# Optimization experiments

Measured on AMD Instinct MI355X. Metric: run time of the kernel, lower is better.

The kernel has to match this reference:

```python
import jax, jax.numpy as jnp
import numpy as np

SEQ, D_IN, D_OUT = 4096, 1024, 1024

def setup_inputs() -> dict:
    key = jax.random.key(0)
    kx, kq, kk, kv = jax.random.split(key, 4)
    s = 1.0 / np.sqrt(D_IN)
    return {
        "x": jax.random.normal(kx, (SEQ, D_IN), dtype=jnp.float32),
        "Wq": jax.random.uniform(kq, (D_IN, D_OUT), dtype=jnp.float32, minval=-s, maxval=s),
        "Wk": jax.random.uniform(kk, (D_IN, D_OUT), dtype=jnp.float32, minval=-s, maxval=s),
        "Wv": jax.random.uniform(kv, (D_IN, D_OUT), dtype=jnp.float32, minval=-s, maxval=s),
    }

def reference(x, Wq, Wk, Wv):
    # Single-head self-attention on a 2-D input [S, d_in].
    q = x @ Wq  # [S, d_out]
    k = x @ Wk
    v = x @ Wv
    scale = 1.0 / jnp.sqrt(jnp.asarray(k.shape[-1], dtype=q.dtype))
    attn = jax.nn.softmax(jnp.einsum('sd,td->st', q, k) * scale, axis=-1)  # [S, S]
    return attn @ v  # [S, d_out]
```

## Files before the change

kernel.cpp:

```cpp
#include <hip/hip_runtime.h>
#include <stdint.h>

typedef __bf16 bf16;
typedef __bf16 bf16x8 __attribute__((ext_vector_type(8)));
typedef __bf16 bf16x4 __attribute__((ext_vector_type(4)));
typedef float  f32x4  __attribute__((ext_vector_type(4)));

#define DEVINL __device__ __forceinline__

DEVINL void gload_lds16(const void* g, void* l) {
  __builtin_amdgcn_global_load_lds(
      (const __attribute__((address_space(1))) uint32_t*)g,
      (__attribute__((address_space(3))) uint32_t*)l, 16, 0, 0);
}

DEVINL void swizzle_xy(int& bx, int& by) {
  const int gx = gridDim.x, gy = gridDim.y;
  const int nwg = gx * gy;
  int lin = blockIdx.y * gx + blockIdx.x;
  if ((nwg & 7) == 0) lin = (lin & 7) * (nwg >> 3) + (lin >> 3);
  bx = lin % gx; by = lin / gx;
}

template<int SWM>
DEVINL int swz(int r) { return ((r ^ (r >> 2)) & SWM) << 4; }

template<int BM, int BN, int BK>
DEVINL void gemm_core(const bf16* __restrict__ A, const bf16* __restrict__ Bt,
                      int K, int row0, int col0,
                      bf16* As, bf16* Bs, f32x4 (&acc)[BM/32][BN/32])
{
  constexpr int FM = BM / 32, FN = BN / 32;
  constexpr int RB  = BK * 2;
  constexpr int SWM = (RB / 16) - 1 > 7 ? 7 : (RB / 16) - 1;
  constexpr int IA  = BM * RB / 4096;
  constexpr int IB  = BN * RB / 4096;
  constexpr int RPI = 4096 / RB;
  constexpr int ABY = BM * BK * 2;
  constexpr int BBY = BN * BK * 2;
  const int tid = threadIdx.x;
  const int wave = tid >> 6, lane = tid & 63;

  const int sL   = tid * 16;
  const int srow = sL / RB;
  const int scb  = (sL % RB) ^ swz<SWM>(srow);
  const bf16* gA = A  + (size_t)(row0 + srow) * K + (scb >> 1);
  const bf16* gB = Bt + (size_t)(col0 + srow) * K + (scb >> 1);

  const int wr = (wave >> 1) * (BM / 2);
  const int wc = (wave & 1)  * (BN / 2);
  const int fr = lane & 15, kg16 = (lane >> 4) * 16;

  #pragma unroll
  for (int i = 0; i < FM; i++)
    #pragma unroll
    for (int j = 0; j < FN; j++)
      acc[i][j] = f32x4{0.f, 0.f, 0.f, 0.f};

  auto stage = [&](int buf, int ti) {
    const bf16* ga = gA + (size_t)ti * BK;
    const bf16* gb = gB + (size_t)ti * BK;
    #pragma unroll
    for (int i = 0; i < IA; i++)
      gload_lds16(ga + (size_t)i * RPI * K, (char*)As + buf * ABY + i * 4096 + sL);
    #pragma unroll
    for (int i = 0; i < IB; i++)
      gload_lds16(gb + (size_t)i * RPI * K, (char*)Bs + buf * BBY + i * 4096 + sL);
  };

  const int nt = K / BK;
  stage(0, 0);
  __syncthreads();
  int cur = 0;
  for (int ti = 0; ti < nt; ++ti) {
    if (ti + 1 < nt) stage(cur ^ 1, ti + 1);
    const char* aB = (const char*)As + cur * ABY;
    const char* bB = (const char*)Bs + cur * BBY;
    #pragma unroll
    for (int kk = 0; kk < BK / 32; ++kk) {
      bf16x8 af[FM], bg[FN];
      #pragma unroll
      for (int m = 0; m < FM; m++) {
        const int r = wr + fr + m * 16;
        af[m] = *(const bf16x8*)(aB + r * RB + ((kk * 64 + kg16) ^ swz<SWM>(r)));
      }
      #pragma unroll
      for (int n = 0; n < FN; n++) {
        const int r = wc + fr + n * 16;
        bg[n] = *(const bf16x8*)(bB + r * RB + ((kk * 64 + kg16) ^ swz<SWM>(r)));
      }
      #pragma unroll
      for (int m = 0; m < FM; m++)
        #pragma unroll
        for (int n = 0; n < FN; n++)
          acc[m][n] = __builtin_amdgcn_mfma_f32_16x16x32_bf16(af[m], bg[n], acc[m][n], 0, 0, 0);
    }
    __syncthreads();
    cur ^= 1;
  }
}

template<int BM, int BN, int BK, int MODE>
__global__ __launch_bounds__(256)
void gemm_bt(const bf16* __restrict__ A, const bf16* __restrict__ Bt,
             void* __restrict__ Cout, int K, int ldc)
{
  __shared__ __align__(16) bf16 As[2 * BM * BK];
  __shared__ __align__(16) bf16 Bs[2 * BN * BK];
  int bx, by; swizzle_xy(bx, by);
  const int row0 = by * BM, col0 = bx * BN;
  f32x4 acc[BM / 32][BN / 32];
  gemm_core<BM, BN, BK>(A, Bt, K, row0, col0, As, Bs, acc);

  const int wave = threadIdx.x >> 6, lane = threadIdx.x & 63;
  const int wr = (wave >> 1) * (BM / 2), wc = (wave & 1) * (BN / 2);
  const int ec = lane & 15, er = (lane >> 4) * 4;
  #pragma unroll
  for (int m = 0; m < BM / 32; m++)
    #pragma unroll
    for (int n = 0; n < BN / 32; n++) {
      const int r = row0 + wr + m * 16 + er;
      const int c = col0 + wc + n * 16 + ec;
      if constexpr (MODE == 0) {
        bf16* C = (bf16*)Cout;
        #pragma unroll
        for (int j = 0; j < 4; j++)
          C[(size_t)(r + j) * ldc + c] = (bf16)acc[m][n][j];
      } else {
        float* C = (float*)Cout;
        #pragma unroll
        for (int j = 0; j < 4; j++)
          C[(size_t)(r + j) * ldc + c] = acc[m][n][j];
      }
    }
}

__global__ __launch_bounds__(256)
void gemm_qkv(const bf16* __restrict__ xb, const bf16* __restrict__ Wt,
              bf16* __restrict__ Qb, bf16* __restrict__ Kb, bf16* __restrict__ Vt)
{
  __shared__ __align__(16) bf16 As[2 * 128 * 32];
  __shared__ __align__(16) bf16 Bs[2 * 128 * 32];
  const int z = blockIdx.z;
  int bx, by; swizzle_xy(bx, by);
  const int row0 = by * 128, col0 = bx * 128;
  f32x4 acc[4][4];
  gemm_core<128, 128, 32>(xb, Wt + (size_t)z * 1024 * 1024, 1024, row0, col0, As, Bs, acc);

  const int wave = threadIdx.x >> 6, lane = threadIdx.x & 63;
  const int wr = (wave >> 1) * 64, wc = (wave & 1) * 64;
  const int ec = lane & 15, er = (lane >> 4) * 4;
  if (z == 2) {
    #pragma unroll
    for (int m = 0; m < 4; m++)
      #pragma unroll
      for (int n = 0; n < 4; n++) {
        const int r = row0 + wr + m * 16 + er;
        const int c = col0 + wc + n * 16 + ec;
        bf16x4 pk;
        #pragma unroll
        for (int j = 0; j < 4; j++) pk[j] = (bf16)acc[m][n][j];
        *(bf16x4*)(Vt + (size_t)c * 4096 + r) = pk;
      }
  } else {
    bf16* C = z ? Kb : Qb;
    const float sc = z ? 1.0f : 0.03125f;
    #pragma unroll
    for (int m = 0; m < 4; m++)
      #pragma unroll
      for (int n = 0; n < 4; n++) {
        const int r = row0 + wr + m * 16 + er;
        const int c = col0 + wc + n * 16 + ec;
        #pragma unroll
        for (int j = 0; j < 4; j++)
          C[(size_t)(r + j) * 1024 + c] = (bf16)(acc[m][n][j] * sc);
      }
  }
}

__global__ __launch_bounds__(256)
void softmax_inplace(bf16* __restrict__ S)
{
  const int t = threadIdx.x;
  bf16* p = S + (size_t)blockIdx.x * 4096 + t * 16;
  bf16x8 v0 = *(const bf16x8*)p;
  bf16x8 v1 = *(const bf16x8*)(p + 8);
  float f[16];
  #pragma unroll
  for (int j = 0; j < 8; j++) { f[j] = (float)v0[j]; f[8 + j] = (float)v1[j]; }
  float mx = f[0];
  #pragma unroll
  for (int j = 1; j < 16; j++) mx = fmaxf(mx, f[j]);
  #pragma unroll
  for (int off = 32; off > 0; off >>= 1) mx = fmaxf(mx, __shfl_xor(mx, off));
  __shared__ float rmax[4], rsum[4];
  const int wave = t >> 6, lane = t & 63;
  if (lane == 0) rmax[wave] = mx;
  __syncthreads();
  mx = fmaxf(fmaxf(rmax[0], rmax[1]), fmaxf(rmax[2], rmax[3]));
  float s = 0.f;
  #pragma unroll
  for (int j = 0; j < 16; j++) { f[j] = __expf(f[j] - mx); s += f[j]; }
  #pragma unroll
  for (int off = 32; off > 0; off >>= 1) s += __shfl_xor(s, off);
  if (lane == 0) rsum[wave] = s;
  __syncthreads();
  const float inv = 1.f / (rsum[0] + rsum[1] + rsum[2] + rsum[3]);
  #pragma unroll
  for (int j = 0; j < 8; j++) {
    v0[j] = (bf16)(f[j] * inv);
    v1[j] = (bf16)(f[8 + j] * inv);
  }
  *(bf16x8*)p = v0;
  *(bf16x8*)(p + 8) = v1;
}

__global__ __launch_bounds__(256)
void cvt_f32_bf16(const float* __restrict__ in, bf16* __restrict__ o)
{
  const size_t i = ((size_t)blockIdx.x * 256 + threadIdx.x) * 8;
  const float4 a = *(const float4*)(in + i);
  const float4 b = *(const float4*)(in + i + 4);
  bf16x8 v;
  v[0] = (bf16)a.x; v[1] = (bf16)a.y; v[2] = (bf16)a.z; v[3] = (bf16)a.w;
  v[4] = (bf16)b.x; v[5] = (bf16)b.y; v[6] = (bf16)b.z; v[7] = (bf16)b.w;
  *(bf16x8*)(o + i) = v;
}

__global__ __launch_bounds__(256)
void transpose_cvt(const float* __restrict__ Wq, const float* __restrict__ Wk,
                   const float* __restrict__ Wv, bf16* __restrict__ Wt)
{
  const float* W = blockIdx.z == 0 ? Wq : (blockIdx.z == 1 ? Wk : Wv);
  bf16* O = Wt + (size_t)blockIdx.z * 1024 * 1024;
  __shared__ bf16 tile[64][65];
  const int tx = threadIdx.x & 63;
  const int tg = threadIdx.x >> 6;
  const int r0 = blockIdx.y * 64;
  const int c0 = blockIdx.x * 64;
  #pragma unroll
  for (int i = 0; i < 16; i++) {
    const int r = i * 4 + tg;
    tile[tx][r] = (bf16)W[(size_t)(r0 + r) * 1024 + c0 + tx];
  }
  __syncthreads();
  #pragma unroll
  for (int i = 0; i < 16; i++) {
    const int rr = i * 4 + tg;
    O[(size_t)(c0 + rr) * 1024 + r0 + tx] = tile[rr][tx];
  }
}

extern "C" void kernel_launch(void* const* d_in, const int* in_sizes, int n_in,
                              void* d_out, int out_size, void* d_ws, size_t ws_size,
                              hipStream_t stream)
{
  const float* x  = (const float*)d_in[0];
  const float* Wq = (const float*)d_in[1];
  const float* Wk = (const float*)d_in[2];
  const float* Wv = (const float*)d_in[3];
  char* ws = (char*)d_ws;
  const size_t MB = 1024 * 1024;
  bf16* xb = (bf16*)(ws);
  bf16* Wt = (bf16*)(ws +  8 * MB);
  bf16* Qb = (bf16*)(ws + 14 * MB);
  bf16* Kb = (bf16*)(ws + 22 * MB);
  bf16* Vt = (bf16*)(ws + 30 * MB);
  bf16* S  = (bf16*)(ws + 38 * MB);

  cvt_f32_bf16   <<<dim3(2048),      dim3(256), 0, stream>>>(x, xb);
  transpose_cvt  <<<dim3(16, 16, 3), dim3(256), 0, stream>>>(Wq, Wk, Wv, Wt);
  gemm_qkv       <<<dim3(8, 32, 3),  dim3(256), 0, stream>>>(xb, Wt, Qb, Kb, Vt);
  gemm_bt<128, 128, 32, 0><<<dim3(32, 32), dim3(256), 0, stream>>>(Qb, Kb, (void*)S, 1024, 4096);
  softmax_inplace<<<dim3(4096),      dim3(256), 0, stream>>>(S);
  gemm_bt<128, 64, 64, 1><<<dim3(16, 32), dim3(256), 0, stream>>>(S, Vt, (void*)d_out, 4096, 1024);
}
```

Baseline: 221.9 us.

## Use 256x256-tile 8-wave pipelined GEMM for QKV projection and QK^T

Adds a new GEMM core with 256x256 output tiles, 512 threads (8 waves), K-tile 64, and a double-buffered direct-to-LDS load schedule. The per-half loads are interleaved with four MFMA quadrant phases, separated by explicit barriers and s_setprio. The QKV projection and the Q·K^T score GEMM both switch to this kernel, and QKV is launched as one 12x16 grid over the concatenated weights. The aim is more data reuse per tile and overlap of global loads with MFMA work. The cost is far fewer workgroups (192 and 256) plus heavy register and 128KB LDS use, which can leave CUs underfilled.

```diff
diff --git a/kernel.cpp b/kernel.cpp
--- a/kernel.cpp
+++ b/kernel.cpp
@@ -7,6 +7,8 @@
 typedef float  f32x4  __attribute__((ext_vector_type(4)));
 
 #define DEVINL __device__ __forceinline__
+#define BAR()    asm volatile("s_barrier" ::: "memory")
+#define WAITV(n) asm volatile("s_waitcnt vmcnt(" #n ")" ::: "memory")
 
 DEVINL void gload_lds16(const void* g, void* l) {
   __builtin_amdgcn_global_load_lds(
@@ -20,6 +22,166 @@
   int lin = blockIdx.y * gx + blockIdx.x;
   if ((nwg & 7) == 0) lin = (lin & 7) * (nwg >> 3) + (lin >> 3);
   bx = lin % gx; by = lin / gx;
+}
+
+DEVINL void gemm8_core(const bf16* __restrict__ A, const bf16* __restrict__ Bt,
+                       int row0, int col0, char* Asm, char* Bsm,
+                       f32x4 (&acc)[8][4])
+{
+  const int t = threadIdx.x;
+  const int wave = t >> 6, lane = t & 63;
+  const int wm = wave >> 2, wn = wave & 3;
+  const int wmBase = wm * 128, wnBase = wn * 64;
+  const int fr = lane & 15, kg16 = (lane >> 4) * 16;
+  const int fsw = (fr & 7) << 4;
+
+  const int sL   = t * 16;
+  const int srow = t >> 3;
+  const int scb  = ((t & 7) << 4) ^ ((srow & 7) << 4);
+  const bf16* Ag = A  + (size_t)(row0 + srow) * 1024 + (scb >> 1);
+  const bf16* Bg = Bt + (size_t)(col0 + srow) * 1024 + (scb >> 1);
+
+  bf16x8 aF[4][2], bF[4][2];
+
+  #pragma unroll
+  for (int i = 0; i < 8; i++)
+    #pragma unroll
+    for (int j = 0; j < 4; j++)
+      acc[i][j] = f32x4{0.f, 0.f, 0.f, 0.f};
+
+  auto stA = [&](int buf, int kt2, int h) {
+    const bf16* g = Ag + (size_t)h * 131072 + kt2 * 64;
+    char* l = Asm + buf * 32768 + h * 16384 + sL;
+    gload_lds16(g, l);
+    gload_lds16(g + 65536, l + 8192);
+  };
+  auto stB = [&](int buf, int kt2, int h) {
+    const bf16* g = Bg + (size_t)h * 131072 + kt2 * 64;
+    char* l = Bsm + buf * 32768 + h * 16384 + sL;
+    gload_lds16(g, l);
+    gload_lds16(g + 65536, l + 8192);
+  };
+  auto rdA = [&](const char* cA, int qm) {
+    #pragma unroll
+    for (int m = 0; m < 4; m++)
+      #pragma unroll
+      for (int kk = 0; kk < 2; kk++)
+        aF[m][kk] = *(const bf16x8*)(cA + (wmBase + qm * 64 + m * 16 + fr) * 128
+                                        + (((kk << 6) + kg16) ^ fsw));
+  };
+  auto rdB = [&](const char* cB, int qn) {
+    #pragma unroll
+    for (int n = 0; n < 2; n++)
+      #pragma unroll
+      for (int kk = 0; kk < 2; kk++)
+        bF[qn * 2 + n][kk] = *(const bf16x8*)(cB + (wnBase + qn * 32 + n * 16 + fr) * 128
+                                                 + (((kk << 6) + kg16) ^ fsw));
+  };
+  auto quad = [&](int qm, int qn) {
+    #pragma unroll
+    for (int m = 0; m < 4; m++)
+      #pragma unroll
+      for (int n = 0; n < 2; n++)
+        #pragma unroll
+        for (int kk = 0; kk < 2; kk++)
+          acc[qm * 4 + m][qn * 2 + n] = __builtin_amdgcn_mfma_f32_16x16x32_bf16(
+              aF[m][kk], bF[qn * 2 + n][kk], acc[qm * 4 + m][qn * 2 + n], 0, 0, 0);
+  };
+
+  stB(0, 0, 0); stA(0, 0, 0); stA(0, 0, 1); stB(0, 0, 1);
+  stB(1, 1, 0); stA(1, 1, 0);
+  WAITV(4); BAR();
+
+  #pragma unroll 1
+  for (int kt = 0; kt < 16; ++kt) {
+    const int cur = kt & 1, oth = cur ^ 1;
+    const char* cA = Asm + cur * 32768;
+    const char* cB = Bsm + cur * 32768;
+    rdA(cA, 0); rdB(cB, 0);
+    if (kt + 1 < 16) stA(oth, kt + 1, 1);
+    BAR(); __builtin_amdgcn_s_setprio(1); quad(0, 0); __builtin_amdgcn_s_setprio(0); BAR();
+    rdB(cB, 1);
+    if (kt + 1 < 16) stB(oth, kt + 1, 1);
+    BAR(); __builtin_amdgcn_s_setprio(1); quad(0, 1); __builtin_amdgcn_s_setprio(0); BAR();
+    rdA(cA, 1);
+    if (kt + 2 < 16) stB(cur, kt + 2, 0);
+    BAR(); __builtin_amdgcn_s_setprio(1); quad(1, 1); __builtin_amdgcn_s_setprio(0); BAR();
+    if (kt + 2 < 16) stA(cur, kt + 2, 0);
+    BAR(); __builtin_amdgcn_s_setprio(1); quad(1, 0); __builtin_amdgcn_s_setprio(0);
+    if (kt < 14)       { WAITV(4); }
+    else if (kt == 14) { WAITV(0); }
+    BAR();
+  }
+}
+
+__global__ __launch_bounds__(512, 2)
+void gemm8_s(const bf16* __restrict__ Qb, const bf16* __restrict__ Kb,
+             bf16* __restrict__ S)
+{
+  __shared__ __align__(16) char Asm[65536];
+  __shared__ __align__(16) char Bsm[65536];
+  int bx, by; swizzle_xy(bx, by);
+  const int row0 = by * 256, col0 = bx * 256;
+  f32x4 acc[8][4];
+  gemm8_core(Qb, Kb, row0, col0, Asm, Bsm, acc);
+
+  const int wave = threadIdx.x >> 6, lane = threadIdx.x & 63;
+  const int wm = wave >> 2, wn = wave & 3;
+  const int ec = lane & 15, er = (lane >> 4) * 4;
+  #pragma unroll
+  for (int m = 0; m < 8; m++)
+    #pragma unroll
+    for (int n = 0; n < 4; n++) {
+      const int r = row0 + wm * 128 + m * 16 + er;
+      const int c = col0 + wn * 64 + n * 16 + ec;
+      #pragma unroll
+      for (int j = 0; j < 4; j++)
+        S[(size_t)(r + j) * 4096 + c] = (bf16)acc[m][n][j];
+    }
+}
+
+__global__ __launch_bounds__(512, 2)
+void gemm8_qkv(const bf16* __restrict__ xb, const bf16* __restrict__ Wt,
+               bf16* __restrict__ Qb, bf16* __restrict__ Kb, bf16* __restrict__ Vt)
+{
+  __shared__ __align__(16) char Asm[65536];
+  __shared__ __align__(16) char Bsm[65536];
+  int bx, by; swizzle_xy(bx, by);
+  const int row0 = by * 256, col0 = bx * 256;
+  f32x4 acc[8][4];
+  gemm8_core(xb, Wt, row0, col0, Asm, Bsm, acc);
+
+  const int wave = threadIdx.x >> 6, lane = threadIdx.x & 63;
+  const int wm = wave >> 2, wn = wave & 3;
+  const int ec = lane & 15, er = (lane >> 4) * 4;
+  const int mid = col0 >> 10;
+  const int cl0 = col0 & 1023;
+  if (mid == 2) {
+    #pragma unroll
+    for (int m = 0; m < 8; m++)
+      #pragma unroll
+      for (int n = 0; n < 4; n++) {
+        const int r = row0 + wm * 128 + m * 16 + er;
+        const int c = cl0 + wn * 64 + n * 16 + ec;
+        bf16x4 pk;
+        #pragma unroll
+        for (int j = 0; j < 4; j++) pk[j] = (bf16)acc[m][n][j];
+        *(bf16x4*)(Vt + (size_t)c * 4096 + r) = pk;
+      }
+  } else {
+    bf16* C = mid ? Kb : Qb;
+    const float sc = mid ? 1.0f : 0.03125f;
+    #pragma unroll
+    for (int m = 0; m < 8; m++)
+      #pragma unroll
+      for (int n = 0; n < 4; n++) {
+        const int r = row0 + wm * 128 + m * 16 + er;
+        const int c = cl0 + wn * 64 + n * 16 + ec;
+        #pragma unroll
+        for (int j = 0; j < 4; j++)
+          C[(size_t)(r + j) * 1024 + c] = (bf16)(acc[m][n][j] * sc);
+      }
+  }
 }
 
 template<int SWM>
@@ -100,10 +262,10 @@
   }
 }
 
-template<int BM, int BN, int BK, int MODE>
+template<int BM, int BN, int BK>
 __global__ __launch_bounds__(256)
 void gemm_bt(const bf16* __restrict__ A, const bf16* __restrict__ Bt,
-             void* __restrict__ Cout, int K, int ldc)
+             float* __restrict__ C, int K, int ldc)
 {
   __shared__ __align__(16) bf16 As[2 * BM * BK];
   __shared__ __align__(16) bf16 Bs[2 * BN * BK];
@@ -121,61 +283,10 @@
     for (int n = 0; n < BN / 32; n++) {
       const int r = row0 + wr + m * 16 + er;
       const int c = col0 + wc + n * 16 + ec;
-      if constexpr (MODE == 0) {
-        bf16* C = (bf16*)Cout;
-        #pragma unroll
-        for (int j = 0; j < 4; j++)
-          C[(size_t)(r + j) * ldc + c] = (bf16)acc[m][n][j];
-      } else {
-        float* C = (float*)Cout;
-        #pragma unroll
-        for (int j = 0; j < 4; j++)
-          C[(size_t)(r + j) * ldc + c] = acc[m][n][j];
-      }
+      #pragma unroll
+      for (int j = 0; j < 4; j++)
+        C[(size_t)(r + j) * ldc + c] = acc[m][n][j];
     }
-}
-
-__global__ __launch_bounds__(256)
-void gemm_qkv(const bf16* __restrict__ xb, const bf16* __restrict__ Wt,
-              bf16* __restrict__ Qb, bf16* __restrict__ Kb, bf16* __restrict__ Vt)
-{
-  __shared__ __align__(16) bf16 As[2 * 128 * 32];
-  __shared__ __align__(16) bf16 Bs[2 * 128 * 32];
-  const int z = blockIdx.z;
-  int bx, by; swizzle_xy(bx, by);
-  const int row0 = by * 128, col0 = bx * 128;
-  f32x4 acc[4][4];
-  gemm_core<128, 128, 32>(xb, Wt + (size_t)z * 1024 * 1024, 1024, row0, col0, As, Bs, acc);
-
-  const int wave = threadIdx.x >> 6, lane = threadIdx.x & 63;
-  const int wr = (wave >> 1) * 64, wc = (wave & 1) * 64;
-  const int ec = lane & 15, er = (lane >> 4) * 4;
-  if (z == 2) {
-    #pragma unroll
-    for (int m = 0; m < 4; m++)
-      #pragma unroll
-      for (int n = 0; n < 4; n++) {
-        const int r = row0 + wr + m * 16 + er;
-        const int c = col0 + wc + n * 16 + ec;
-        bf16x4 pk;
-        #pragma unroll
-        for (int j = 0; j < 4; j++) pk[j] = (bf16)acc[m][n][j];
-        *(bf16x4*)(Vt + (size_t)c * 4096 + r) = pk;
-      }
-  } else {
-    bf16* C = z ? Kb : Qb;
-    const float sc = z ? 1.0f : 0.03125f;
-    #pragma unroll
-    for (int m = 0; m < 4; m++)
-      #pragma unroll
-      for (int n = 0; n < 4; n++) {
-        const int r = row0 + wr + m * 16 + er;
-        const int c = col0 + wc + n * 16 + ec;
-        #pragma unroll
-        for (int j = 0; j < 4; j++)
-          C[(size_t)(r + j) * 1024 + c] = (bf16)(acc[m][n][j] * sc);
-      }
-  }
 }
 
 __global__ __launch_bounds__(256)
@@ -270,8 +381,8 @@
 
   cvt_f32_bf16   <<<dim3(2048),      dim3(256), 0, stream>>>(x, xb);
   transpose_cvt  <<<dim3(16, 16, 3), dim3(256), 0, stream>>>(Wq, Wk, Wv, Wt);
-  gemm_qkv       <<<dim3(8, 32, 3),  dim3(256), 0, stream>>>(xb, Wt, Qb, Kb, Vt);
-  gemm_bt<128, 128, 32, 0><<<dim3(32, 32), dim3(256), 0, stream>>>(Qb, Kb, (void*)S, 1024, 4096);
+  gemm8_qkv      <<<dim3(12, 16),    dim3(512), 0, stream>>>(xb, Wt, Qb, Kb, Vt);
+  gemm8_s        <<<dim3(16, 16),    dim3(512), 0, stream>>>(Qb, Kb, S);
   softmax_inplace<<<dim3(4096),      dim3(256), 0, stream>>>(S);
-  gemm_bt<128, 64, 64, 1><<<dim3(16, 32), dim3(256), 0, stream>>>(S, Vt, (void*)d_out, 4096, 1024);
-}
+  gemm_bt<128, 64, 64><<<dim3(16, 32), dim3(256), 0, stream>>>(S, Vt, (float*)d_out, 4096, 1024);
+}
```

Result: faster. 207.6 us (-6.4%).
